# Performance work log

Measured on AMD Instinct MI355X. Metric: run time of the kernel, lower is better.

Reference implementation:

```python
import jax, jax.numpy as jnp
import numpy as np

B, S, IN, OUT = 4, 8192, 768, 768
ALPHA = 0.01


def setup_inputs() -> dict:
    key = jax.random.key(0)
    kx, kw, kb = jax.random.split(key, 3)
    x = jax.random.randint(kx, (B, S, IN), -127, 127, dtype=jnp.int8)
    weight = jax.random.randint(kw, (IN, OUT), -127, 127, dtype=jnp.int8)
    bias = (jax.random.normal(kb, (1, OUT), dtype=jnp.float32) * 0.1).astype(jnp.float16)
    alpha = jnp.float32(ALPHA)
    return {"x": x, "weight": weight, "bias": bias, "alpha": alpha}


def reference(x, weight, bias, alpha):
    # x: [B, S, IN] int8, weight: [IN, OUT] int8 (Conv1D layout), bias: [1, OUT] fp16
    x_shape = x.shape
    xf = x.reshape(-1, x_shape[-1])                      # [N, IN] int8

    # rand_elements = zeros of x dtype (int8) -> masked_x == x, but keep the
    # wrap-bit detection chain faithful to the source.
    rand_elements = jnp.zeros_like(xf)                   # int8 zeros
    masked_x = xf + rand_elements                        # int8 wraparound add
    m32 = masked_x.astype(jnp.int32)
    x32 = xf.astype(jnp.int32)
    r32 = rand_elements.astype(jnp.int32)
    wraps = ((m32 ^ x32) & (m32 ^ r32) & 128) >> 7       # [N, IN] int32 (all zero here)
    wraps = jnp.where((wraps < 0) & (m32 < 0), 1, wraps)
    wraps = wraps.astype(jnp.int8)

    wf = weight.astype(jnp.float32)                      # [IN, OUT]
    # F.linear(masked_x.float(), weight.t().float()) == masked_x @ weight
    hidden = masked_x.astype(jnp.float32) @ wf           # [N, OUT] fp32
    overflow = ((wraps.astype(jnp.float32) @ wf).astype(jnp.int32) << 8)
    hidden = hidden + overflow.astype(jnp.float32)

    mask_mul = jnp.zeros((xf.shape[0], OUT), dtype=jnp.float32)
    y = hidden - mask_mul
    fp_y = y * alpha + bias.astype(jnp.float32)          # dequant scale + bias
    yq = jnp.clip(jnp.round(fp_y), -128, 127).astype(jnp.int8)
    return yq.reshape(*x_shape[:-1], -1)
```

## Files before the change

kernel.cpp:

```cpp
#include <hip/hip_runtime.h>

#define M_TOT 32768
#define K_TOT 768
#define N_TOT 768

typedef int v4i __attribute__((ext_vector_type(4)));

#define GLOAD_LDS(g, l) __builtin_amdgcn_global_load_lds( \
    (const __attribute__((address_space(1))) unsigned int*)(g), \
    (__attribute__((address_space(3))) unsigned int*)(l), 16, 0, 0)

__device__ __forceinline__ unsigned pack4(v4i a) {
  unsigned lo = __builtin_amdgcn_perm((unsigned)a.y, (unsigned)a.x, 0x00000400u);
  unsigned hi = __builtin_amdgcn_perm((unsigned)a.w, (unsigned)a.z, 0x00000400u);
  return __builtin_amdgcn_perm(hi, lo, 0x05040100u);
}

__global__ __launch_bounds__(256) void pack_w_kernel(const int* __restrict__ W,
                                                     signed char* __restrict__ W8T) {
  __shared__ signed char t[64][72];
  const int k0 = blockIdx.x * 64, n0 = blockIdx.y * 64;
  for (int i = threadIdx.x; i < 4096; i += 256) {
    int k = i >> 6, n = i & 63;
    t[n][k] = (signed char)W[(k0 + k) * N_TOT + n0 + n];
  }
  __syncthreads();
  for (int i = threadIdx.x; i < 4096; i += 256) {
    int n = i >> 6, k = i & 63;
    W8T[(n0 + n) * K_TOT + k0 + k] = t[n][k];
  }
}

__global__ __launch_bounds__(512, 4) void gemm_i8_kernel(
    const int* __restrict__ X, const signed char* __restrict__ W8T,
    const float* __restrict__ bias, const float* __restrict__ alpha_p,
    int* __restrict__ out) {
  __shared__ __align__(16) signed char Abuf[2][8192];
  __shared__ __align__(16) signed char Bbuf[2][8192];

  const int d = blockIdx.x;
  const int t = (d & 7) * 192 + (d >> 3);
  const int mt = t / 6, nt = t - mt * 6;
  const int row0 = mt << 7, col0 = nt << 7;

  const int tid = threadIdx.x;
  const int lane = tid & 63;
  const int wave = tid >> 6;
  const int wr = wave >> 1, wc = wave & 1;
  const int fr = lane & 15, fg = lane >> 4;
  const int fsw = (fr & 3) << 4;

  const int arow = tid >> 4;
  const int acol = (tid & 15) << 2;
  const int* Xbase = X + (row0 + arow) * K_TOT + acol;
  const int awsw = (arow & 3) << 4;

  const int bsrc = (col0 + (tid >> 2)) * K_TOT +
                   (((tid & 3) << 4) ^ (((tid >> 2) & 3) << 4));
  const int bdst = wave * 1024;

  v4i q[4];
  const v4i zero = {0, 0, 0, 0};
  v4i acc[2][4];
#pragma unroll
  for (int m = 0; m < 2; ++m)
#pragma unroll
    for (int n = 0; n < 4; ++n) acc[m][n] = zero;

#define ISSUE_A(ks)                                                      \
  do {                                                                   \
    const int* _p = Xbase + (ks) * 64;                                   \
    _Pragma("unroll") for (int j = 0; j < 4; ++j)                        \
        q[j] = *(const v4i*)(_p + j * 32 * K_TOT);                       \
  } while (0)

#define ISSUE_B(ks)                                                      \
  GLOAD_LDS(W8T + (ks) * 64 + bsrc, &Bbuf[(ks) & 1][bdst])

#define PACK_WRITE_A(tt)                                                 \
  do {                                                                   \
    signed char* _ab = Abuf[(tt) & 1];                                   \
    _Pragma("unroll") for (int j = 0; j < 4; ++j) {                      \
      unsigned _dw = pack4(q[j]);                                        \
      *(unsigned*)&_ab[(32 * j + arow) * 64 + (acol ^ awsw)] = _dw;      \
    }                                                                    \
  } while (0)

#define FRAGS_MFMA(ks)                                                   \
  do {                                                                   \
    v4i af[2], bf[4];                                                    \
    const signed char* _ab = Abuf[(ks) & 1];                             \
    const signed char* _bb = Bbuf[(ks) & 1];                             \
    const int _kb = (fg << 4) ^ fsw;                                     \
    _Pragma("unroll") for (int m = 0; m < 2; ++m)                        \
        af[m] = *(const v4i*)&_ab[(wr * 32 + m * 16 + fr) * 64 + _kb];   \
    _Pragma("unroll") for (int n = 0; n < 4; ++n)                        \
        bf[n] = *(const v4i*)&_bb[(wc * 64 + n * 16 + fr) * 64 + _kb];   \
    __builtin_amdgcn_s_setprio(1);                                       \
    _Pragma("unroll") for (int m = 0; m < 2; ++m)                        \
        _Pragma("unroll") for (int n = 0; n < 4; ++n)                    \
            acc[m][n] = __builtin_amdgcn_mfma_i32_16x16x64_i8(           \
                af[m], bf[n], acc[m][n], 0, 0, 0);                       \
    __builtin_amdgcn_s_setprio(0);                                       \
  } while (0)

#define GITER(ks, TOPW)                                                  \
  do {                                                                   \
    asm volatile("s_waitcnt vmcnt(" TOPW ") lgkmcnt(0)" ::: "memory");   \
    __builtin_amdgcn_s_barrier();                                        \
    if ((ks) + 1 < 12) ISSUE_B((ks) + 1);                                \
    FRAGS_MFMA(ks);                                                      \
    if ((ks) + 1 < 12) {                                                 \
      asm volatile("s_waitcnt vmcnt(1)" ::: "memory");                   \
      PACK_WRITE_A((ks) + 1);                                            \
      if ((ks) + 2 < 12) ISSUE_A((ks) + 2);                              \
    }                                                                    \
  } while (0)

  ISSUE_A(0);
  ISSUE_B(0);
  asm volatile("s_waitcnt vmcnt(1)" ::: "memory");
  PACK_WRITE_A(0);
  ISSUE_A(1);

  GITER(0, "4");
  GITER(1, "4");
  GITER(2, "4");
  GITER(3, "4");
  GITER(4, "4");
  GITER(5, "4");
  GITER(6, "4");
  GITER(7, "4");
  GITER(8, "4");
  GITER(9, "4");
  GITER(10, "4");
  GITER(11, "0");

  const float alpha = *alpha_p;
  float bv[4];
#pragma unroll
  for (int n = 0; n < 4; ++n) bv[n] = bias[col0 + wc * 64 + n * 16 + fr];

#pragma unroll
  for (int m = 0; m < 2; ++m) {
    int orow = row0 + wr * 32 + m * 16 + fg * 4;
#pragma unroll
    for (int n = 0; n < 4; ++n) {
      int ocol = col0 + wc * 64 + n * 16 + fr;
      int* po = out + orow * N_TOT + ocol;
#pragma unroll
      for (int r = 0; r < 4; ++r) {
        float v = rintf((float)acc[m][n][r] * alpha + bv[n]);
        v = fminf(127.f, fmaxf(-128.f, v));
        po[r * N_TOT] = (int)v;
      }
    }
  }
}

extern "C" void kernel_launch(void* const* d_in, const int* in_sizes, int n_in,
                              void* d_out, int out_size, void* d_ws, size_t ws_size,
                              hipStream_t stream) {
  const int* X = (const int*)d_in[0];
  const int* W = (const int*)d_in[1];
  const float* bias = (const float*)d_in[2];
  const float* alpha = (const float*)d_in[3];
  int* out = (int*)d_out;
  signed char* W8T = (signed char*)d_ws;

  dim3 pg(K_TOT / 64, N_TOT / 64);
  pack_w_kernel<<<pg, 256, 0, stream>>>(W, W8T);
  gemm_i8_kernel<<<(M_TOT / 128) * (N_TOT / 128), 512, 0, stream>>>(X, W8T, bias, alpha, out);
}
```

Measured before the change: 58.47 us.

## Double K-step to 128, triple-buffer B tiles, and vectorize A packing

Each pipeline stage now covers a K slice of 128 instead of 64, which halves the number of barrier iterations. B tiles are triple-buffered so the weight prefetch runs two stages ahead. Each thread now packs eight int32 vectors from one row into two 16-byte LDS stores instead of four scattered dword stores, using an 8-way XOR swizzle. The cost is more LDS per block (80KB versus 32KB), which may limit occupancy below the requested 4 blocks per CU, and more registers for the q buffers.

```diff
diff --git a/kernel.cpp b/kernel.cpp
--- a/kernel.cpp
+++ b/kernel.cpp
@@ -5,6 +5,7 @@
 #define N_TOT 768
 
 typedef int v4i __attribute__((ext_vector_type(4)));
+typedef unsigned int v4u __attribute__((ext_vector_type(4)));
 
 #define GLOAD_LDS(g, l) __builtin_amdgcn_global_load_lds( \
     (const __attribute__((address_space(1))) unsigned int*)(g), \
@@ -35,8 +36,8 @@
     const int* __restrict__ X, const signed char* __restrict__ W8T,
     const float* __restrict__ bias, const float* __restrict__ alpha_p,
     int* __restrict__ out) {
-  __shared__ __align__(16) signed char Abuf[2][8192];
-  __shared__ __align__(16) signed char Bbuf[2][8192];
+  __shared__ __align__(16) signed char Abuf[2][16384];
+  __shared__ __align__(16) signed char Bbuf[3][16384];
 
   const int d = blockIdx.x;
   const int t = (d & 7) * 192 + (d >> 3);
@@ -48,18 +49,25 @@
   const int wave = tid >> 6;
   const int wr = wave >> 1, wc = wave & 1;
   const int fr = lane & 15, fg = lane >> 4;
-  const int fsw = (fr & 3) << 4;
+  const int fsw = (fr & 7) << 4;
 
-  const int arow = tid >> 4;
-  const int acol = (tid & 15) << 2;
-  const int* Xbase = X + (row0 + arow) * K_TOT + acol;
-  const int awsw = (arow & 3) << 4;
+  const int arow = tid >> 2;
+  const int acolw = (tid & 3) << 5;
+  const int* Xbase = X + (row0 + arow) * K_TOT + acolw;
+  const int awsw = (arow & 7) << 4;
+  const int aoff0 = arow * 128 + ((acolw + 0) ^ awsw);
+  const int aoff1 = arow * 128 + ((acolw + 16) ^ awsw);
 
-  const int bsrc = (col0 + (tid >> 2)) * K_TOT +
-                   (((tid & 3) << 4) ^ (((tid >> 2) & 3) << 4));
-  const int bdst = wave * 1024;
+  int bsrc[2], bdst[2];
+#pragma unroll
+  for (int h = 0; h < 2; ++h) {
+    int c = h * 512 + tid;
+    int r = c >> 3, slot = c & 7;
+    bsrc[h] = (col0 + r) * K_TOT + ((slot << 4) ^ ((r & 7) << 4));
+    bdst[h] = h * 8192 + wave * 1024;
+  }
 
-  v4i q[4];
+  v4i q[8];
   const v4i zero = {0, 0, 0, 0};
   v4i acc[2][4];
 #pragma unroll
@@ -69,33 +77,40 @@
 
 #define ISSUE_A(ks)                                                      \
   do {                                                                   \
-    const int* _p = Xbase + (ks) * 64;                                   \
-    _Pragma("unroll") for (int j = 0; j < 4; ++j)                        \
-        q[j] = *(const v4i*)(_p + j * 32 * K_TOT);                       \
+    const int* _p = Xbase + (ks) * 128;                                  \
+    _Pragma("unroll") for (int j = 0; j < 8; ++j)                        \
+        q[j] = *(const v4i*)(_p + ((j & 3) << 2) + ((j >> 2) << 4));     \
   } while (0)
 
 #define ISSUE_B(ks)                                                      \
-  GLOAD_LDS(W8T + (ks) * 64 + bsrc, &Bbuf[(ks) & 1][bdst])
-
-#define PACK_WRITE_A(tt)                                                 \
   do {                                                                   \
-    signed char* _ab = Abuf[(tt) & 1];                                   \
-    _Pragma("unroll") for (int j = 0; j < 4; ++j) {                      \
-      unsigned _dw = pack4(q[j]);                                        \
-      *(unsigned*)&_ab[(32 * j + arow) * 64 + (acol ^ awsw)] = _dw;      \
-    }                                                                    \
+    const signed char* _w = W8T + (ks) * 128;                            \
+    signed char* _lb = Bbuf[(ks) % 3];                                   \
+    GLOAD_LDS(_w + bsrc[0], _lb + bdst[0]);                              \
+    GLOAD_LDS(_w + bsrc[1], _lb + bdst[1]);                              \
   } while (0)
 
-#define FRAGS_MFMA(ks)                                                   \
+#define PACK_WRITE_A(ss)                                                 \
+  do {                                                                   \
+    signed char* _ab = Abuf[(ss) & 1];                                   \
+    unsigned _pk[8];                                                     \
+    _Pragma("unroll") for (int j = 0; j < 8; ++j) _pk[j] = pack4(q[j]);  \
+    v4u _w0 = {_pk[0], _pk[1], _pk[2], _pk[3]};                          \
+    v4u _w1 = {_pk[4], _pk[5], _pk[6], _pk[7]};                          \
+    *(v4u*)&_ab[aoff0] = _w0;                                            \
+    *(v4u*)&_ab[aoff1] = _w1;                                            \
+  } while (0)
+
+#define FRAGS_K(ks, kk)                                                  \
   do {                                                                   \
     v4i af[2], bf[4];                                                    \
     const signed char* _ab = Abuf[(ks) & 1];                             \
-    const signed char* _bb = Bbuf[(ks) & 1];                             \
-    const int _kb = (fg << 4) ^ fsw;                                     \
+    const signed char* _bb = Bbuf[(ks) % 3];                             \
+    const int _kb = ((kk) * 64 + fg * 16) ^ fsw;                         \
     _Pragma("unroll") for (int m = 0; m < 2; ++m)                        \
-        af[m] = *(const v4i*)&_ab[(wr * 32 + m * 16 + fr) * 64 + _kb];   \
+        af[m] = *(const v4i*)&_ab[(wr * 32 + m * 16 + fr) * 128 + _kb];  \
     _Pragma("unroll") for (int n = 0; n < 4; ++n)                        \
-        bf[n] = *(const v4i*)&_bb[(wc * 64 + n * 16 + fr) * 64 + _kb];   \
+        bf[n] = *(const v4i*)&_bb[(wc * 64 + n * 16 + fr) * 128 + _kb];  \
     __builtin_amdgcn_s_setprio(1);                                       \
     _Pragma("unroll") for (int m = 0; m < 2; ++m)                        \
         _Pragma("unroll") for (int n = 0; n < 4; ++n)                    \
@@ -104,37 +119,33 @@
     __builtin_amdgcn_s_setprio(0);                                       \
   } while (0)
 
-#define GITER(ks, TOPW)                                                  \
+#define GITER(ks, TOPW, MIDW, DOB, DOA, DOPACK)                          \
   do {                                                                   \
     asm volatile("s_waitcnt vmcnt(" TOPW ") lgkmcnt(0)" ::: "memory");   \
     __builtin_amdgcn_s_barrier();                                        \
-    if ((ks) + 1 < 12) ISSUE_B((ks) + 1);                                \
-    FRAGS_MFMA(ks);                                                      \
-    if ((ks) + 1 < 12) {                                                 \
-      asm volatile("s_waitcnt vmcnt(1)" ::: "memory");                   \
+    if (DOB) ISSUE_B((ks) + 2);                                          \
+    FRAGS_K(ks, 0);                                                      \
+    if (DOPACK) {                                                        \
+      asm volatile("s_waitcnt vmcnt(" MIDW ")" ::: "memory");            \
       PACK_WRITE_A((ks) + 1);                                            \
-      if ((ks) + 2 < 12) ISSUE_A((ks) + 2);                              \
+      if (DOA) ISSUE_A((ks) + 2);                                        \
     }                                                                    \
+    FRAGS_K(ks, 1);                                                      \
   } while (0)
 
   ISSUE_A(0);
   ISSUE_B(0);
-  asm volatile("s_waitcnt vmcnt(1)" ::: "memory");
+  ISSUE_B(1);
+  asm volatile("s_waitcnt vmcnt(4)" ::: "memory");
   PACK_WRITE_A(0);
   ISSUE_A(1);
 
-  GITER(0, "4");
-  GITER(1, "4");
-  GITER(2, "4");
-  GITER(3, "4");
-  GITER(4, "4");
-  GITER(5, "4");
-  GITER(6, "4");
-  GITER(7, "4");
-  GITER(8, "4");
-  GITER(9, "4");
-  GITER(10, "4");
-  GITER(11, "0");
+  GITER(0, "10", "2", 1, 1, 1);
+  GITER(1, "10", "2", 1, 1, 1);
+  GITER(2, "10", "2", 1, 1, 1);
+  GITER(3, "10", "2", 1, 1, 1);
+  GITER(4, "10", "0", 0, 0, 1);
+  GITER(5, "0", "0", 0, 0, 0);
 
   const float alpha = *alpha_p;
   float bv[4];
```

New measurement: 92.65 us. 1.58x slower.

## Shrink GEMM tile to 64x64, load A fragments directly into registers, 4-stage B ring

Applied to the files above, without the earlier changes.

Each block now computes a 64x64 tile with 256 threads. Every wave loads its own 16 rows of the int32 activations straight into registers and packs them into MFMA A fragments, so the LDS staging of A and its write/read are removed. Weight tiles go through a 4-buffer LDS ring with loads issued three k-steps ahead. The cost is four times as many blocks, each fetching the same W tiles and A rows more often with less reuse, and more registers held for the in-flight A loads.

```diff
diff --git a/kernel.cpp b/kernel.cpp
--- a/kernel.cpp
+++ b/kernel.cpp
@@ -31,129 +31,95 @@
   }
 }
 
-__global__ __launch_bounds__(512, 4) void gemm_i8_kernel(
+__global__ __launch_bounds__(256, 4) void gemm_i8_kernel(
     const int* __restrict__ X, const signed char* __restrict__ W8T,
     const float* __restrict__ bias, const float* __restrict__ alpha_p,
     int* __restrict__ out) {
-  __shared__ __align__(16) signed char Abuf[2][8192];
-  __shared__ __align__(16) signed char Bbuf[2][8192];
+  __shared__ __align__(16) signed char Bbuf[4][4096];
 
   const int d = blockIdx.x;
-  const int t = (d & 7) * 192 + (d >> 3);
-  const int mt = t / 6, nt = t - mt * 6;
-  const int row0 = mt << 7, col0 = nt << 7;
+  const int t = (d & 7) * 768 + (d >> 3);
+  const int mt = t / 12, nt = t - mt * 12;
+  const int row0 = mt << 6, col0 = nt << 6;
 
   const int tid = threadIdx.x;
   const int lane = tid & 63;
-  const int wave = tid >> 6;
-  const int wr = wave >> 1, wc = wave & 1;
+  const int wv = tid >> 6;
   const int fr = lane & 15, fg = lane >> 4;
-  const int fsw = (fr & 3) << 4;
 
-  const int arow = tid >> 4;
-  const int acol = (tid & 15) << 2;
-  const int* Xbase = X + (row0 + arow) * K_TOT + acol;
-  const int awsw = (arow & 3) << 4;
+  const int* Xrow = X + (row0 + wv * 16 + fr) * K_TOT + fg * 16;
 
   const int bsrc = (col0 + (tid >> 2)) * K_TOT +
                    (((tid & 3) << 4) ^ (((tid >> 2) & 3) << 4));
-  const int bdst = wave * 1024;
 
-  v4i q[4];
+  const int brd = fr * 64 + ((fg << 4) ^ ((fr & 3) << 4));
+
+  v4i q[3][4];
   const v4i zero = {0, 0, 0, 0};
-  v4i acc[2][4];
+  v4i acc[4];
 #pragma unroll
-  for (int m = 0; m < 2; ++m)
-#pragma unroll
-    for (int n = 0; n < 4; ++n) acc[m][n] = zero;
+  for (int n = 0; n < 4; ++n) acc[n] = zero;
 
 #define ISSUE_A(ks)                                                      \
   do {                                                                   \
-    const int* _p = Xbase + (ks) * 64;                                   \
     _Pragma("unroll") for (int j = 0; j < 4; ++j)                        \
-        q[j] = *(const v4i*)(_p + j * 32 * K_TOT);                       \
+        q[(ks) % 3][j] = *(const v4i*)(Xrow + (ks) * 64 + j * 4);        \
   } while (0)
 
 #define ISSUE_B(ks)                                                      \
-  GLOAD_LDS(W8T + (ks) * 64 + bsrc, &Bbuf[(ks) & 1][bdst])
+  GLOAD_LDS(W8T + (ks) * 64 + bsrc, &Bbuf[(ks) & 3][wv * 1024])
 
-#define PACK_WRITE_A(tt)                                                 \
+#define GITER(ks, TOPW, DO3)                                             \
   do {                                                                   \
-    signed char* _ab = Abuf[(tt) & 1];                                   \
-    _Pragma("unroll") for (int j = 0; j < 4; ++j) {                      \
-      unsigned _dw = pack4(q[j]);                                        \
-      *(unsigned*)&_ab[(32 * j + arow) * 64 + (acol ^ awsw)] = _dw;      \
-    }                                                                    \
-  } while (0)
-
-#define FRAGS_MFMA(ks)                                                   \
-  do {                                                                   \
-    v4i af[2], bf[4];                                                    \
-    const signed char* _ab = Abuf[(ks) & 1];                             \
-    const signed char* _bb = Bbuf[(ks) & 1];                             \
-    const int _kb = (fg << 4) ^ fsw;                                     \
-    _Pragma("unroll") for (int m = 0; m < 2; ++m)                        \
-        af[m] = *(const v4i*)&_ab[(wr * 32 + m * 16 + fr) * 64 + _kb];   \
+    asm volatile("s_waitcnt vmcnt(" TOPW ")" ::: "memory");              \
+    __builtin_amdgcn_s_barrier();                                        \
+    v4i af;                                                              \
+    af.x = (int)pack4(q[(ks) % 3][0]);                                   \
+    af.y = (int)pack4(q[(ks) % 3][1]);                                   \
+    af.z = (int)pack4(q[(ks) % 3][2]);                                   \
+    af.w = (int)pack4(q[(ks) % 3][3]);                                   \
+    if (DO3) { ISSUE_B((ks) + 3); ISSUE_A((ks) + 3); }                   \
+    v4i bf[4];                                                           \
     _Pragma("unroll") for (int n = 0; n < 4; ++n)                        \
-        bf[n] = *(const v4i*)&_bb[(wc * 64 + n * 16 + fr) * 64 + _kb];   \
+        bf[n] = *(const v4i*)&Bbuf[(ks) & 3][n * 1024 + brd];            \
     __builtin_amdgcn_s_setprio(1);                                       \
-    _Pragma("unroll") for (int m = 0; m < 2; ++m)                        \
-        _Pragma("unroll") for (int n = 0; n < 4; ++n)                    \
-            acc[m][n] = __builtin_amdgcn_mfma_i32_16x16x64_i8(           \
-                af[m], bf[n], acc[m][n], 0, 0, 0);                       \
+    _Pragma("unroll") for (int n = 0; n < 4; ++n)                        \
+        acc[n] = __builtin_amdgcn_mfma_i32_16x16x64_i8(af, bf[n],        \
+                                                       acc[n], 0, 0, 0); \
     __builtin_amdgcn_s_setprio(0);                                       \
   } while (0)
 
-#define GITER(ks, TOPW)                                                  \
-  do {                                                                   \
-    asm volatile("s_waitcnt vmcnt(" TOPW ") lgkmcnt(0)" ::: "memory");   \
-    __builtin_amdgcn_s_barrier();                                        \
-    if ((ks) + 1 < 12) ISSUE_B((ks) + 1);                                \
-    FRAGS_MFMA(ks);                                                      \
-    if ((ks) + 1 < 12) {                                                 \
-      asm volatile("s_waitcnt vmcnt(1)" ::: "memory");                   \
-      PACK_WRITE_A((ks) + 1);                                            \
-      if ((ks) + 2 < 12) ISSUE_A((ks) + 2);                              \
-    }                                                                    \
-  } while (0)
+  ISSUE_B(0); ISSUE_A(0);
+  ISSUE_B(1); ISSUE_A(1);
+  ISSUE_B(2); ISSUE_A(2);
 
-  ISSUE_A(0);
-  ISSUE_B(0);
-  asm volatile("s_waitcnt vmcnt(1)" ::: "memory");
-  PACK_WRITE_A(0);
-  ISSUE_A(1);
-
-  GITER(0, "4");
-  GITER(1, "4");
-  GITER(2, "4");
-  GITER(3, "4");
-  GITER(4, "4");
-  GITER(5, "4");
-  GITER(6, "4");
-  GITER(7, "4");
-  GITER(8, "4");
-  GITER(9, "4");
-  GITER(10, "4");
-  GITER(11, "0");
+  GITER(0, "10", 1);
+  GITER(1, "10", 1);
+  GITER(2, "10", 1);
+  GITER(3, "10", 1);
+  GITER(4, "10", 1);
+  GITER(5, "10", 1);
+  GITER(6, "10", 1);
+  GITER(7, "10", 1);
+  GITER(8, "10", 1);
+  GITER(9, "10", 0);
+  GITER(10, "5", 0);
+  GITER(11, "0", 0);
 
   const float alpha = *alpha_p;
   float bv[4];
 #pragma unroll
-  for (int n = 0; n < 4; ++n) bv[n] = bias[col0 + wc * 64 + n * 16 + fr];
+  for (int n = 0; n < 4; ++n) bv[n] = bias[col0 + n * 16 + fr];
 
+  const int orow0 = row0 + wv * 16 + fg * 4;
 #pragma unroll
-  for (int m = 0; m < 2; ++m) {
-    int orow = row0 + wr * 32 + m * 16 + fg * 4;
+  for (int n = 0; n < 4; ++n) {
+    int* po = out + orow0 * N_TOT + col0 + n * 16 + fr;
 #pragma unroll
-    for (int n = 0; n < 4; ++n) {
-      int ocol = col0 + wc * 64 + n * 16 + fr;
-      int* po = out + orow * N_TOT + ocol;
-#pragma unroll
-      for (int r = 0; r < 4; ++r) {
-        float v = rintf((float)acc[m][n][r] * alpha + bv[n]);
-        v = fminf(127.f, fmaxf(-128.f, v));
-        po[r * N_TOT] = (int)v;
-      }
+    for (int r = 0; r < 4; ++r) {
+      float v = rintf((float)acc[n][r] * alpha + bv[n]);
+      v = fminf(127.f, fmaxf(-128.f, v));
+      po[r * N_TOT] = (int)v;
     }
   }
 }
@@ -170,5 +136,5 @@
 
   dim3 pg(K_TOT / 64, N_TOT / 64);
   pack_w_kernel<<<pg, 256, 0, stream>>>(W, W8T);
-  gemm_i8_kernel<<<(M_TOT / 128) * (N_TOT / 128), 512, 0, stream>>>(X, W8T, bias, alpha, out);
+  gemm_i8_kernel<<<(M_TOT / 64) * (N_TOT / 64), 256, 0, stream>>>(X, W8T, bias, alpha, out);
 }
```

Measured after the change: 154.5 us. +164.3%, slower.
